# Performance work log

Measured on AMD Instinct MI355X. Metric: run time of the kernel, lower is better.

## Reference

```python
import jax, jax.numpy as jnp
import numpy as np

B, T, L = 256, 1024, 64
INIT = 0.1


def setup_inputs() -> dict:
    key = jax.random.key(0)
    k1, k2, k3, k4, k5 = jax.random.split(key, 5)
    scores = jax.random.normal(k1, (B, T, L), dtype=jnp.float32)
    targets = jax.random.randint(k2, (B, T), 0, L)
    start = jax.random.uniform(k3, (L,), dtype=jnp.float32, minval=-INIT, maxval=INIT)
    T_mat = jax.random.uniform(k4, (L, L), dtype=jnp.float32, minval=-INIT, maxval=INIT)
    end = jax.random.uniform(k5, (L,), dtype=jnp.float32, minval=-INIT, maxval=INIT)
    return {"scores": scores, "targets": targets, "start": start, "T_mat": T_mat, "end": end}


def reference(scores, targets, start, T_mat, end):
    # scores: [B,T,L], targets: [B,T] int, start/end: [L], T_mat: [L,L] with T_mat[cur, prev]
    Ttr = T_mat.T  # [prev, cur]

    # --- normalizers via forward algorithm (scan over time) ---
    prev0 = start[None, :] + scores[:, 0]  # [B,L]

    def step(prev, emit):  # prev [B,L], emit [B,L]
        cur = prev[:, :, None] + emit[:, None, :] + Ttr[None, :, :]  # [B,prev,cur]
        return jax.scipy.special.logsumexp(cur, axis=1), None

    emits_t = jnp.swapaxes(scores, 0, 1)[1:]  # [T-1,B,L]
    prev, _ = jax.lax.scan(step, prev0, emits_t)
    normalizers = jax.scipy.special.logsumexp(prev + end[None, :], axis=1)  # [B]

    # --- gold path score ---
    emits = jnp.take_along_axis(scores, targets[:, :, None], axis=2).squeeze(2).sum(axis=1)  # [B]
    trans = (start[targets[:, 0]]
             + T_mat[targets[:, 1:], targets[:, :-1]].sum(axis=1)
             + end[targets[:, -1]])  # [B]
    target_scores = emits + trans

    return (normalizers - target_scores).mean()
```

## Files before the change

kernel.cpp:

```cpp
#include <hip/hip_runtime.h>

#define NB 256
#define NT 1024
#define NL 64

typedef __fp16 h2v __attribute__((ext_vector_type(2)));

__device__ __forceinline__ float rfl_f(float v) {
  return __builtin_bit_cast(float, __builtin_amdgcn_readfirstlane(__builtin_bit_cast(int, v)));
}

__device__ __forceinline__ float dpp_xor1(float v) {
  int i = __builtin_bit_cast(int, v);
  int r = __builtin_amdgcn_update_dpp(i, i, 0xB1, 0xF, 0xF, false);
  return __builtin_bit_cast(float, r);
}

#define CRF_DOT8(K0)                                                          \
  do {                                                                        \
    int b0 = __builtin_amdgcn_readlane(pki, 2 * (K0 + 0));                    \
    int b1 = __builtin_amdgcn_readlane(pki, 2 * (K0 + 1));                    \
    int b2 = __builtin_amdgcn_readlane(pki, 2 * (K0 + 2));                    \
    int b3 = __builtin_amdgcn_readlane(pki, 2 * (K0 + 3));                    \
    int b4 = __builtin_amdgcn_readlane(pki, 2 * (K0 + 4));                    \
    int b5 = __builtin_amdgcn_readlane(pki, 2 * (K0 + 5));                    \
    int b6 = __builtin_amdgcn_readlane(pki, 2 * (K0 + 6));                    \
    int b7 = __builtin_amdgcn_readlane(pki, 2 * (K0 + 7));                    \
    s0 = __builtin_amdgcn_fdot2(__builtin_bit_cast(h2v, b0), Rh[K0 + 0], s0, false); \
    s1 = __builtin_amdgcn_fdot2(__builtin_bit_cast(h2v, b1), Rh[K0 + 1], s1, false); \
    s2 = __builtin_amdgcn_fdot2(__builtin_bit_cast(h2v, b2), Rh[K0 + 2], s2, false); \
    s3 = __builtin_amdgcn_fdot2(__builtin_bit_cast(h2v, b3), Rh[K0 + 3], s3, false); \
    s0 = __builtin_amdgcn_fdot2(__builtin_bit_cast(h2v, b4), Rh[K0 + 4], s0, false); \
    s1 = __builtin_amdgcn_fdot2(__builtin_bit_cast(h2v, b5), Rh[K0 + 5], s1, false); \
    s2 = __builtin_amdgcn_fdot2(__builtin_bit_cast(h2v, b6), Rh[K0 + 6], s2, false); \
    s3 = __builtin_amdgcn_fdot2(__builtin_bit_cast(h2v, b7), Rh[K0 + 7], s3, false); \
  } while (0)

#define CRF_STEP(EF)                                                          \
  do {                                                                        \
    float pn = dpp_xor1(p);                                                   \
    h2v pk = __builtin_amdgcn_cvt_pkrtz(p, pn);                               \
    int pki = __builtin_bit_cast(int, pk);                                    \
    float s0 = 0.f, s1 = 0.f, s2 = 0.f, s3 = 0.f;                             \
    CRF_DOT8(0);                                                              \
    CRF_DOT8(8);                                                              \
    CRF_DOT8(16);                                                             \
    CRF_DOT8(24);                                                             \
    float u = ((s0 + s1) + (s2 + s3)) * (EF);                                 \
    int ub = __builtin_amdgcn_readfirstlane(__builtin_bit_cast(int, u));      \
    int eb = (ub >> 23) & 0xff;                                               \
    p = u * __builtin_bit_cast(float, (252 - eb) << 23);                      \
    e2 += eb - 125;                                                           \
  } while (0)

__global__ __launch_bounds__(64) void fb_kernel(const float* __restrict__ scores,
                                                const int* __restrict__ targets,
                                                const float* __restrict__ start,
                                                const float* __restrict__ Tm,
                                                const float* __restrict__ endv,
                                                float* __restrict__ wsA,
                                                float* __restrict__ wsB,
                                                float* __restrict__ wsG) {
  const int lane = threadIdx.x;
  const int bb = blockIdx.x;

  if (bb >= 2 * NB) {
    const int b = bb - 2 * NB;
    const int* tg = targets + b * NT;
    const float* sc = scores + (size_t)b * NT * NL;
    float acc = 0.f;
    for (int t = lane; t < NT; t += 64) {
      int c = tg[t];
      acc += sc[t * NL + c];
      if (t > 0) acc += Tm[c * NL + tg[t - 1]];
    }
#pragma unroll
    for (int off = 32; off > 0; off >>= 1) acc += __shfl_xor(acc, off, 64);
    if (lane == 0) wsG[b] = acc + start[tg[0]] + endv[tg[NT - 1]];
    return;
  }

  const bool bwd = bb >= NB;
  const int b = bwd ? bb - NB : bb;
  const float* sc = scores + (size_t)b * NT * NL;
  const float LN2 = 0.69314718055994530942f;

  const float* Tb = bwd ? (Tm + lane) : (Tm + lane * NL);
  const int str = bwd ? NL : 1;
  h2v Rh[32];
#pragma unroll
  for (int k = 0; k < 32; k++)
    Rh[k] = __builtin_amdgcn_cvt_pkrtz(__expf(Tb[(2 * k) * str]),
                                       __expf(Tb[(2 * k + 1) * str]));

  if (!bwd) {
    float a0 = start[lane] + sc[lane];
    float m0 = rfl_f(a0);
    float p = __expf(a0 - m0) * 0.25f;
    int e2 = 2;

    float buf[4];
#pragma unroll
    for (int k = 0; k < 4; k++) buf[k] = sc[(1 + k) * NL + lane];

    for (int i = 0; i < 128; i++) {
      float nb4[4];
      int tb = 5 + 4 * i;
#pragma unroll
      for (int k = 0; k < 4; k++) nb4[k] = sc[(tb + k) * NL + lane];
      float Ev[4];
#pragma unroll
      for (int k = 0; k < 4; k++) Ev[k] = __expf(buf[k]);
      CRF_STEP(Ev[0]);
      CRF_STEP(Ev[1]);
      CRF_STEP(Ev[2]);
      CRF_STEP(Ev[3]);
#pragma unroll
      for (int k = 0; k < 4; k++) buf[k] = nb4[k];
    }
    wsA[lane * NB + b] = m0 + (float)e2 * LN2 + __logf(p);
  } else {
    float a0 = endv[lane] + sc[(NT - 1) * NL + lane];
    float m0 = rfl_f(a0);
    float p = __expf(a0 - m0) * 0.25f;
    int e2 = 2;

    float buf[4];
#pragma unroll
    for (int k = 0; k < 4; k++) buf[k] = sc[(1022 - k) * NL + lane];

    for (int i = 0; i < 127; i++) {
      float nb4[4];
      int tb = 1018 - 4 * i;
#pragma unroll
      for (int k = 0; k < 4; k++) nb4[k] = sc[(tb - k) * NL + lane];
      float Ev[4];
#pragma unroll
      for (int k = 0; k < 4; k++) Ev[k] = __expf(buf[k]);
      CRF_STEP(Ev[0]);
      CRF_STEP(Ev[1]);
      CRF_STEP(Ev[2]);
      CRF_STEP(Ev[3]);
#pragma unroll
      for (int k = 0; k < 4; k++) buf[k] = nb4[k];
    }
    CRF_STEP(__expf(sc[514 * NL + lane]));
    CRF_STEP(__expf(sc[513 * NL + lane]));
    CRF_STEP(1.0f);
    wsB[lane * NB + b] = m0 + (float)e2 * LN2 + __logf(p);
  }
}

__global__ __launch_bounds__(256) void combine_kernel(const float* __restrict__ wsA,
                                                      const float* __restrict__ wsB,
                                                      const float* __restrict__ wsG,
                                                      float* __restrict__ out) {
  const int b = threadIdx.x;
  float m = -INFINITY;
#pragma unroll
  for (int j = 0; j < NL; j++) m = fmaxf(m, wsA[j * NB + b] + wsB[j * NB + b]);
  float s = 0.f;
#pragma unroll
  for (int j = 0; j < NL; j++) s += __expf(wsA[j * NB + b] + wsB[j * NB + b] - m);
  float loss = (m + __logf(s)) - wsG[b];
#pragma unroll
  for (int off = 32; off > 0; off >>= 1) loss += __shfl_xor(loss, off, 64);
  __shared__ float red[4];
  if ((b & 63) == 0) red[b >> 6] = loss;
  __syncthreads();
  if (b == 0) out[0] = (red[0] + red[1] + red[2] + red[3]) * (1.0f / NB);
}

extern "C" void kernel_launch(void* const* d_in, const int* in_sizes, int n_in,
                              void* d_out, int out_size, void* d_ws, size_t ws_size,
                              hipStream_t stream) {
  const float* scores = (const float*)d_in[0];
  const int* targets = (const int*)d_in[1];
  const float* start = (const float*)d_in[2];
  const float* Tm = (const float*)d_in[3];
  const float* endv = (const float*)d_in[4];
  float* out = (float*)d_out;

  float* wsA = (float*)d_ws;
  float* wsB = wsA + NB * NL;
  float* wsG = wsB + NB * NL;

  fb_kernel<<<3 * NB, 64, 0, stream>>>(scores, targets, start, Tm, endv, wsA, wsB, wsG);
  combine_kernel<<<1, 256, 0, stream>>>(wsA, wsB, wsG, out);
}
```

Baseline: 181.6 us.

## Broadcast packed state through LDS vector loads instead of per-lane readlane

Each step writes its packed fp16 pair into shared memory and reads the whole 64-value state back as eight int4 broadcast loads, replacing 32 scalar readlane operations per step. The renormalization now takes the exponent of the fp16 value in lane 0 from the loaded data and applies it to the next step's emission factor, removing the readfirstlane on the critical path. In exchange it adds LDS store/load latency and a reliance on in-wave ordering without barriers. Scaling now rests on fp16 exponent bits, which narrows the headroom before overflow or underflow.

```diff
diff --git a/kernel.cpp b/kernel.cpp
--- a/kernel.cpp
+++ b/kernel.cpp
@@ -16,41 +16,27 @@
   return __builtin_bit_cast(float, r);
 }
 
-#define CRF_DOT8(K0)                                                          \
-  do {                                                                        \
-    int b0 = __builtin_amdgcn_readlane(pki, 2 * (K0 + 0));                    \
-    int b1 = __builtin_amdgcn_readlane(pki, 2 * (K0 + 1));                    \
-    int b2 = __builtin_amdgcn_readlane(pki, 2 * (K0 + 2));                    \
-    int b3 = __builtin_amdgcn_readlane(pki, 2 * (K0 + 3));                    \
-    int b4 = __builtin_amdgcn_readlane(pki, 2 * (K0 + 4));                    \
-    int b5 = __builtin_amdgcn_readlane(pki, 2 * (K0 + 5));                    \
-    int b6 = __builtin_amdgcn_readlane(pki, 2 * (K0 + 6));                    \
-    int b7 = __builtin_amdgcn_readlane(pki, 2 * (K0 + 7));                    \
-    s0 = __builtin_amdgcn_fdot2(__builtin_bit_cast(h2v, b0), Rh[K0 + 0], s0, false); \
-    s1 = __builtin_amdgcn_fdot2(__builtin_bit_cast(h2v, b1), Rh[K0 + 1], s1, false); \
-    s2 = __builtin_amdgcn_fdot2(__builtin_bit_cast(h2v, b2), Rh[K0 + 2], s2, false); \
-    s3 = __builtin_amdgcn_fdot2(__builtin_bit_cast(h2v, b3), Rh[K0 + 3], s3, false); \
-    s0 = __builtin_amdgcn_fdot2(__builtin_bit_cast(h2v, b4), Rh[K0 + 4], s0, false); \
-    s1 = __builtin_amdgcn_fdot2(__builtin_bit_cast(h2v, b5), Rh[K0 + 5], s1, false); \
-    s2 = __builtin_amdgcn_fdot2(__builtin_bit_cast(h2v, b6), Rh[K0 + 6], s2, false); \
-    s3 = __builtin_amdgcn_fdot2(__builtin_bit_cast(h2v, b7), Rh[K0 + 7], s3, false); \
-  } while (0)
+#define DOT4(P, B)                                                            \
+  s0 = __builtin_amdgcn_fdot2(__builtin_bit_cast(h2v, (P).x), Rh[(B) + 0], s0, false); \
+  s1 = __builtin_amdgcn_fdot2(__builtin_bit_cast(h2v, (P).y), Rh[(B) + 1], s1, false); \
+  s2 = __builtin_amdgcn_fdot2(__builtin_bit_cast(h2v, (P).z), Rh[(B) + 2], s2, false); \
+  s3 = __builtin_amdgcn_fdot2(__builtin_bit_cast(h2v, (P).w), Rh[(B) + 3], s3, false);
 
 #define CRF_STEP(EF)                                                          \
   do {                                                                        \
-    float pn = dpp_xor1(p);                                                   \
-    h2v pk = __builtin_amdgcn_cvt_pkrtz(p, pn);                               \
-    int pki = __builtin_bit_cast(int, pk);                                    \
+    float wn = dpp_xor1(w);                                                   \
+    h2v pk = __builtin_amdgcn_cvt_pkrtz(w, wn);                               \
+    lb[wslot] = __builtin_bit_cast(int, pk);                                  \
+    int4 P0 = lbv[0], P1 = lbv[1], P2 = lbv[2], P3 = lbv[3];                  \
+    int4 P4 = lbv[4], P5 = lbv[5], P6 = lbv[6], P7 = lbv[7];                  \
+    int e5 = (P0.x >> 10) & 0x1f;                                             \
+    float K = __builtin_bit_cast(float, (130 - e5) << 23);                    \
+    float KE = K * (EF);                                                      \
+    e2 += e5 - 3;                                                             \
     float s0 = 0.f, s1 = 0.f, s2 = 0.f, s3 = 0.f;                             \
-    CRF_DOT8(0);                                                              \
-    CRF_DOT8(8);                                                              \
-    CRF_DOT8(16);                                                             \
-    CRF_DOT8(24);                                                             \
-    float u = ((s0 + s1) + (s2 + s3)) * (EF);                                 \
-    int ub = __builtin_amdgcn_readfirstlane(__builtin_bit_cast(int, u));      \
-    int eb = (ub >> 23) & 0xff;                                               \
-    p = u * __builtin_bit_cast(float, (252 - eb) << 23);                      \
-    e2 += eb - 125;                                                           \
+    DOT4(P0, 0); DOT4(P1, 4); DOT4(P2, 8); DOT4(P3, 12);                      \
+    DOT4(P4, 16); DOT4(P5, 20); DOT4(P6, 24); DOT4(P7, 28);                   \
+    w = ((s0 + s1) + (s2 + s3)) * KE;                                         \
   } while (0)
 
 __global__ __launch_bounds__(64) void fb_kernel(const float* __restrict__ scores,
@@ -80,6 +66,11 @@
     return;
   }
 
+  __shared__ int4 lbv_s[16];
+  int* lb = (int*)lbv_s;
+  const int4* lbv = lbv_s;
+  const int wslot = (lane & 1) * 32 + (lane >> 1);
+
   const bool bwd = bb >= NB;
   const int b = bwd ? bb - NB : bb;
   const float* sc = scores + (size_t)b * NT * NL;
@@ -96,8 +87,8 @@
   if (!bwd) {
     float a0 = start[lane] + sc[lane];
     float m0 = rfl_f(a0);
-    float p = __expf(a0 - m0) * 0.25f;
-    int e2 = 2;
+    float w = __expf(a0 - m0) * 16.f;
+    int e2 = -4;
 
     float buf[4];
 #pragma unroll
@@ -118,12 +109,12 @@
 #pragma unroll
       for (int k = 0; k < 4; k++) buf[k] = nb4[k];
     }
-    wsA[lane * NB + b] = m0 + (float)e2 * LN2 + __logf(p);
+    wsA[lane * NB + b] = m0 + (float)e2 * LN2 + __logf(w);
   } else {
     float a0 = endv[lane] + sc[(NT - 1) * NL + lane];
     float m0 = rfl_f(a0);
-    float p = __expf(a0 - m0) * 0.25f;
-    int e2 = 2;
+    float w = __expf(a0 - m0) * 16.f;
+    int e2 = -4;
 
     float buf[4];
 #pragma unroll
@@ -147,7 +138,7 @@
     CRF_STEP(__expf(sc[514 * NL + lane]));
     CRF_STEP(__expf(sc[513 * NL + lane]));
     CRF_STEP(1.0f);
-    wsB[lane * NB + b] = m0 + (float)e2 * LN2 + __logf(p);
+    wsB[lane * NB + b] = m0 + (float)e2 * LN2 + __logf(w);
   }
 }
 
```

Result: no change. 178.3 us (-1.8%).
